# Performance work log

Hardware: AMD Instinct MI355X
Metric: run time of the kernel (lower is better)

The kernel has to match this reference:

```python
import jax, jax.numpy as jnp
import numpy as np

B, T, N = 256, 512, 256
START, STOP = 254, 255


def setup_inputs() -> dict:
    key = jax.random.key(0)
    k1, k2, k3 = jax.random.split(key, 3)
    inputs = jax.random.normal(k1, (B, T, N), dtype=jnp.float32)
    transitions = jax.random.normal(k2, (N, N), dtype=jnp.float32)
    # sentinel rows/cols as in __init__
    transitions = transitions.at[START, :].set(-10000.0).at[:, STOP].set(-10000.0)
    tags = jax.random.randint(k3, (B, T), 0, N, dtype=jnp.int32)
    mask = jnp.ones((B, T), dtype=jnp.int32)
    return {"inputs": inputs, "transitions": transitions, "tags": tags, "mask": mask}


def _input_likelihood(inputs, transitions, fmask):
    # alpha[b, tag]: log-sum over paths ending at tag
    alpha0 = transitions[:, START][None, :] + inputs[:, 0, :]

    def step(alpha, xs):
        emit, m = xs  # emit: (B, N), m: (B,)
        # inner[b, next, prev] = alpha[b, prev] + (emit[b, next] + trans[next, prev]) * mask[b, i-1]
        inner = alpha[:, None, :] + (emit[:, :, None] + transitions[None, :, :]) * m[:, None, None]
        return jax.nn.logsumexp(inner, axis=-1), None

    xs = (jnp.swapaxes(inputs[:, 1:, :], 0, 1), jnp.swapaxes(fmask[:, :-1], 0, 1))
    alpha, _ = jax.lax.scan(step, alpha0, xs)
    stops = alpha + transitions[STOP][None, :]
    return jax.nn.logsumexp(stops, axis=-1)  # (B,)


def _joint_likelihood(inputs, transitions, tags, fmask):
    score = transitions[tags[:, 0], START]  # (B,)
    # transitions[next, prev] * mask[:, i+1], summed over steps
    trans_sc = transitions[tags[:, 1:], tags[:, :-1]] * fmask[:, 1:]
    # inputs[b, i, prev_tag] * mask[:, i]
    emit_sc = jnp.take_along_axis(inputs[:, :-1, :], tags[:, :-1, None], axis=2)[..., 0] * fmask[:, :-1]
    score = score + trans_sc.sum(axis=-1) + emit_sc.sum(axis=-1)
    last_idx = (fmask.sum(axis=-1) - 1.0).astype(jnp.int32)  # (B,)
    last_tags = jnp.take_along_axis(tags, last_idx[:, None], axis=1)[:, 0]
    last_input = jnp.take_along_axis(inputs[:, -1, :], last_tags[:, None], axis=1)[:, 0]
    return score + transitions[STOP, last_tags] + last_input * fmask[:, -1]


def reference(inputs, transitions, tags, mask):
    fmask = mask.astype(jnp.float32)
    log_denominator = _input_likelihood(inputs, transitions, fmask)
    log_numerator = _joint_likelihood(inputs, transitions, tags, fmask)
    return jnp.sum(log_numerator - log_denominator)
```

## Files before the change

### kernel.cpp

```cpp
#include <hip/hip_runtime.h>
#include <hip/hip_bf16.h>
#include <stdint.h>

#define B_    256
#define T_    512
#define N_    256
#define START_ 254
#define STOP_  255
#define GCOLS 16
#define NF    16
#define ND    32
#define LOG2E 1.4426950408889634f
#define LN2   0.6931471805599453f

#define WSB_OFF 65536
#define WCF_OFF 131072
#define WCB_OFF 131328
#define WNUM_OFF 131584

typedef __attribute__((ext_vector_type(4))) float floatx4;
typedef __attribute__((ext_vector_type(4))) unsigned int uintx4;
typedef __attribute__((ext_vector_type(8))) int v8i;

template<bool X> struct BC { static constexpr bool value = X; };

__device__ __forceinline__ void lds_barrier() {
    asm volatile("s_waitcnt lgkmcnt(0)\n\ts_barrier" ::: "memory");
}
__device__ __forceinline__ float fmax3(float a, float b, float c) {
    return fmaxf(fmaxf(a, b), c);
}
__device__ __forceinline__ uint32_t umax32(uint32_t a, uint32_t b) {
    return a > b ? a : b;
}
__device__ __forceinline__ float pmax16(float x) {
    float a = x, b = x;
    asm("v_permlane16_swap_b32 %0, %1" : "+v"(a), "+v"(b));
    return fmaxf(a, b);
}
__device__ __forceinline__ float pmax32(float x) {
    float a = x, b = x;
    asm("v_permlane32_swap_b32 %0, %1" : "+v"(a), "+v"(b));
    return fmaxf(a, b);
}
__device__ __forceinline__ float psum32(float x) {
    float a = x, b = x;
    asm("v_permlane32_swap_b32 %0, %1" : "+v"(a), "+v"(b));
    return a + b;
}

__device__ __forceinline__ int pk_fp8x4(float a, float b, float c, float d) {
    int r = __builtin_amdgcn_cvt_pk_fp8_f32(a, b, 0, false);
    return __builtin_amdgcn_cvt_pk_fp8_f32(c, d, r, true);
}
__device__ __forceinline__ int pk_bf8x4(float a, float b, float c, float d) {
    int r = __builtin_amdgcn_cvt_pk_bf8_f32(a, b, 0, false);
    return __builtin_amdgcn_cvt_pk_bf8_f32(c, d, r, true);
}

struct DenomShared {
    alignas(16) char  V[2][4096];
    alignas(16) unsigned short mbuf[GCOLS * 8];
    alignas(16) float sbuf[GCOLS * 20];
    int flag;
};

template<bool ISF>
__device__ __forceinline__ void denom_path(
    DenomShared& sh, const float* __restrict__ inputs,
    const float* __restrict__ trans, const int* __restrict__ mask,
    float* __restrict__ ws, int blkLocal)
{
    const int tid = threadIdx.x;
    const int w = tid >> 6;
    const int l = tid & 63;
    const int q = l >> 4;
    const int b = l & 15;
    const int bg = blkLocal * GCOLS + b;
    const int j0 = 32 * w + 4 * q;
    const int S = ISF ? 256 : 255;
    const int scl = 0x7F7F7F7F;

    auto EIDX = [](int s) { return ISF ? s : (511 - s); };
    auto MIDX = [](int s) { return ISF ? (s - 1) : (511 - s); };

    int wa[2];
    #pragma unroll
    for (int mt = 0; mt < 2; ++mt)
        wa[mt] = ((((2 * w + mt) >> 3) * 2 + mt) << 10)
               + ((w & 3) << 8) + (b << 4) + (q << 2);
    const int rbase = l << 4;

    v8i afrag[2][2];
    #pragma unroll
    for (int mt = 0; mt < 2; ++mt) {
        const int row = 32 * w + 16 * mt + b;
        #pragma unroll
        for (int c = 0; c < 2; ++c) {
            v8i a;
            #pragma unroll
            for (int g8 = 0; g8 < 8; ++g8) {
                float e[4];
                if (ISF) {
                    floatx4 t = *(const floatx4*)(trans + row * N_ + c * 128 + q * 32 + 4 * g8);
                    #pragma unroll
                    for (int ii = 0; ii < 4; ++ii)
                        e[ii] = __builtin_amdgcn_exp2f(t[ii] * LOG2E);
                } else {
                    #pragma unroll
                    for (int ii = 0; ii < 4; ++ii) {
                        const int k = c * 128 + q * 32 + 4 * g8 + ii;
                        e[ii] = __builtin_amdgcn_exp2f(trans[k * N_ + row] * LOG2E);
                    }
                }
                a[g8] = pk_fp8x4(e[0], e[1], e[2], e[3]);
            }
            afrag[mt][c] = a;
        }
    }

    {
        const int* mrow = mask + blkLocal * GCOLS * T_;
        bool hd = false;
        #pragma unroll
        for (int i = 0; i < GCOLS * T_ / 512; ++i)
            hd |= (mrow[tid + 512 * i] == 0);
        if (tid == 0) sh.flag = 0;
        __syncthreads();
        if (__any(hd) && l == 0) atomicOr(&sh.flag, 1);
        __syncthreads();
    }
    const bool anyDead = (sh.flag != 0);

    const float* emitp = inputs + (size_t)bg * T_ * N_;
    const int*   maskp = mask + bg * T_;
    int   Ci = 0;
    float u[2][4];

    if (ISF) {
        #pragma unroll
        for (int mt = 0; mt < 2; ++mt) {
            floatx4 em = *(const floatx4*)(emitp + j0 + 16 * mt);
            #pragma unroll
            for (int r = 0; r < 4; ++r) {
                const int j = j0 + 16 * mt + r;
                u[mt][r] = __builtin_amdgcn_exp2f((trans[j * N_ + START_] + em[r]) * LOG2E);
            }
        }
    } else {
        #pragma unroll
        for (int mt = 0; mt < 2; ++mt) {
            floatx4 st = *(const floatx4*)(trans + STOP_ * N_ + j0 + 16 * mt);
            #pragma unroll
            for (int r = 0; r < 4; ++r)
                u[mt][r] = __builtin_amdgcn_exp2f(st[r] * LOG2E);
        }
    }
    {
        float mx = u[0][0], sm = 0.f;
        #pragma unroll
        for (int mt = 0; mt < 2; ++mt)
            #pragma unroll
            for (int r = 0; r < 4; ++r) { mx = fmaxf(mx, u[mt][r]); sm += u[mt][r]; }
        mx = pmax16(mx);
        mx = pmax32(mx);
        if (l < 16)
            sh.mbuf[b * 8 + w] =
                (unsigned short)(__builtin_bit_cast(uint32_t, mx) >> 16);
        sm = psum32(sm);
        if (l < 32) sh.sbuf[b * 20 + w * 2 + q] = sm;

        float xpi[2][4] = {{1.f,1.f,1.f,1.f},{1.f,1.f,1.f,1.f}};
        if (!ISF) {
            #pragma unroll
            for (int mt = 0; mt < 2; ++mt) {
                floatx4 e = *(const floatx4*)(emitp + (size_t)511 * N_ + j0 + 16 * mt);
                #pragma unroll
                for (int r = 0; r < 4; ++r)
                    xpi[mt][r] = __builtin_amdgcn_exp2f(e[r] * LOG2E);
            }
        }
        #pragma unroll
        for (int mt = 0; mt < 2; ++mt)
            *(int*)(sh.V[0] + wa[mt]) =
                pk_bf8x4(u[mt][0] * xpi[mt][0], u[mt][1] * xpi[mt][1],
                         u[mt][2] * xpi[mt][2], u[mt][3] * xpi[mt][3]);
    }

    auto run = [&](auto fastc) {
        constexpr bool FAST = decltype(fastc)::value;
        const long estep = ISF ? (long)N_ : -(long)N_;
        const int  mstep = ISF ? 1 : -1;

        floatx4 xc0, xc1;
        floatx4 rbA0, rbA1;
        floatx4 rbB0, rbB1;
        const float* pe = emitp + (size_t)EIDX(1) * N_ + j0;
        {
            floatx4 e0 = *(const floatx4*)pe;
            floatx4 e1 = *(const floatx4*)(pe + 16);
            pe += estep;
            rbA0 = *(const floatx4*)pe;
            rbA1 = *(const floatx4*)(pe + 16);
            pe += estep;
            rbB0 = *(const floatx4*)pe;
            rbB1 = *(const floatx4*)(pe + 16);
            pe += estep;
            #pragma unroll
            for (int r = 0; r < 4; ++r) {
                xc0[r] = __builtin_amdgcn_exp2f(e0[r] * LOG2E);
                xc1[r] = __builtin_amdgcn_exp2f(e1[r] * LOG2E);
            }
        }
        float mrot[2] = {1.f, 1.f};
        const int* pm = maskp;
        if (!FAST) {
            mrot[0] = (float)maskp[MIDX(1)];
            mrot[1] = (float)maskp[MIDX(2)];
            pm = maskp + MIDX(3);
        }
        lds_barrier();

        auto body = [&](int pr, int cur) {
            const char* vb = sh.V[pr];
            uintx4 r00 = *(const uintx4*)(vb + rbase);
            uintx4 r01 = *(const uintx4*)(vb + 1024 + rbase);
            uintx4 r10 = *(const uintx4*)(vb + 2048 + rbase);
            uintx4 r11 = *(const uintx4*)(vb + 3072 + rbase);
            const uintx4 md = *(const uintx4*)((const uint32_t*)sh.mbuf + b * 4);
            floatx4 eC0 = *(const floatx4*)pe;
            floatx4 eC1 = *(const floatx4*)(pe + 16);
            float mC = 1.f;
            if (!FAST) mC = (float)(*pm);

            floatx4 xn0, xn1;
            #pragma unroll
            for (int r = 0; r < 4; ++r) {
                xn0[r] = __builtin_amdgcn_exp2f(rbA0[r] * LOG2E);
                xn1[r] = __builtin_amdgcn_exp2f(rbA1[r] * LOG2E);
            }

            const uint32_t hm = umax32(umax32(md[0], md[1]), umax32(md[2], md[3]));
            const uint32_t lm = umax32(umax32(md[0] << 16, md[1] << 16),
                                       umax32(md[2] << 16, md[3] << 16));
            const uint32_t mm = umax32(hm, lm);
            const int eb = (int)((mm >> 23) & 0xFFu);
            const float rs = __builtin_bit_cast(float, (uint32_t)(249 - eb) << 23);
            Ci += eb;

            floatx4 rx0, rx1;
            if (ISF) {
                #pragma unroll
                for (int r = 0; r < 4; ++r) { rx0[r] = xc0[r] * rs; rx1[r] = xc1[r] * rs; }
            }

            union { v8i v; struct { uintx4 lo, hi; } p; } bf0, bf1;
            bf0.p.lo = r00; bf0.p.hi = r01;
            bf1.p.lo = r10; bf1.p.hi = r11;

            floatx4 a0 = {0.f,0.f,0.f,0.f}, a1 = {0.f,0.f,0.f,0.f};
            a0 = __builtin_amdgcn_mfma_scale_f32_16x16x128_f8f6f4(
                     afrag[0][0], bf0.v, a0, 0, 1, 0, scl, 0, scl);
            a1 = __builtin_amdgcn_mfma_scale_f32_16x16x128_f8f6f4(
                     afrag[1][0], bf0.v, a1, 0, 1, 0, scl, 0, scl);
            a0 = __builtin_amdgcn_mfma_scale_f32_16x16x128_f8f6f4(
                     afrag[0][1], bf1.v, a0, 0, 1, 0, scl, 0, scl);
            a1 = __builtin_amdgcn_mfma_scale_f32_16x16x128_f8f6f4(
                     afrag[1][1], bf1.v, a1, 0, 1, 0, scl, 0, scl);

            if (FAST) {
                #pragma unroll
                for (int r = 0; r < 4; ++r) {
                    if (ISF) {
                        u[0][r] = a0[r] * rx0[r];
                        u[1][r] = a1[r] * rx1[r];
                    } else {
                        u[0][r] = a0[r] * rs;
                        u[1][r] = a1[r] * rs;
                    }
                }
            } else {
                const bool live = (mrot[cur] != 0.f);
                float csv = 0.f;
                if (__any(!live)) {
                    const float* sb = &sh.sbuf[b * 20];
                    floatx4 s0 = *(const floatx4*)sb,       s1 = *(const floatx4*)(sb + 4);
                    floatx4 s2 = *(const floatx4*)(sb + 8), s3 = *(const floatx4*)(sb + 12);
                    csv = ((((s0[0] + s0[1]) + (s0[2] + s0[3])) +
                            ((s1[0] + s1[1]) + (s1[2] + s1[3]))) +
                           (((s2[0] + s2[1]) + (s2[2] + s2[3])) +
                            ((s3[0] + s3[1]) + (s3[2] + s3[3])))) * rs;
                }
                #pragma unroll
                for (int r = 0; r < 4; ++r) {
                    if (ISF) {
                        u[0][r] = live ? a0[r] * rx0[r] : csv;
                        u[1][r] = live ? a1[r] * rx1[r] : csv;
                    } else {
                        u[0][r] = live ? a0[r] * rs : csv;
                        u[1][r] = live ? a1[r] * rs : csv;
                    }
                }
            }

            {
                float t0 = fmax3(u[0][0], u[0][1], u[0][2]);
                t0 = fmax3(t0, u[0][3], u[1][0]);
                t0 = fmax3(t0, u[1][1], u[1][2]);
                t0 = fmaxf(t0, u[1][3]);
                t0 = pmax16(t0);
                t0 = pmax32(t0);
                if (l < 16)
                    sh.mbuf[b * 8 + w] =
                        (unsigned short)(__builtin_bit_cast(uint32_t, t0) >> 16);
                if (!FAST) {
                    float sm = ((u[0][0] + u[0][1]) + (u[0][2] + u[0][3]))
                             + ((u[1][0] + u[1][1]) + (u[1][2] + u[1][3]));
                    sm = psum32(sm);
                    if (l < 32) sh.sbuf[b * 20 + w * 2 + q] = sm;
                }
            }
            if (ISF) {
                *(int*)(sh.V[pr ^ 1] + wa[0]) = pk_bf8x4(u[0][0], u[0][1], u[0][2], u[0][3]);
                *(int*)(sh.V[pr ^ 1] + wa[1]) = pk_bf8x4(u[1][0], u[1][1], u[1][2], u[1][3]);
            } else {
                *(int*)(sh.V[pr ^ 1] + wa[0]) =
                    pk_bf8x4(u[0][0] * xc0[0], u[0][1] * xc0[1],
                             u[0][2] * xc0[2], u[0][3] * xc0[3]);
                *(int*)(sh.V[pr ^ 1] + wa[1]) =
                    pk_bf8x4(u[1][0] * xc1[0], u[1][1] * xc1[1],
                             u[1][2] * xc1[2], u[1][3] * xc1[3]);
            }
            lds_barrier();
            xc0 = xn0; xc1 = xn1;
            rbA0 = rbB0; rbA1 = rbB1;
            rbB0 = eC0;  rbB1 = eC1;
            pe += estep;
            if (!FAST) { mrot[cur] = mC; pm += mstep; }
        };

        #pragma unroll 1
        for (int g = 0; g < S / 2; ++g) {
            body(0, 0);
            body(1, 1);
        }
        if (S & 1) body(0, 0);
    };

    if (anyDead) run(BC<false>{});
    else         run(BC<true>{});

    float* wsV = ws + (ISF ? 0 : WSB_OFF);
    #pragma unroll
    for (int mt = 0; mt < 2; ++mt) {
        floatx4 vv = {u[mt][0], u[mt][1], u[mt][2], u[mt][3]};
        *(floatx4*)&wsV[(size_t)bg * N_ + j0 + 16 * mt] = vv;
    }
    if (tid < 16) {
        float* wsC = ws + (ISF ? WCF_OFF : WCB_OFF);
        wsC[blkLocal * GCOLS + tid] = (float)(Ci - 122 * S);
    }
}

__global__ __launch_bounds__(512, 2) void crf_main(
    const float* __restrict__ inputs, const float* __restrict__ trans,
    const int* __restrict__ tags, const int* __restrict__ mask,
    float* __restrict__ out, float* __restrict__ ws)
{
    __shared__ DenomShared sh;

    if (blockIdx.x >= ND) {
        float* nred = sh.sbuf;
        int*   nredi = (int*)(sh.sbuf + 8);
        const int bb = blockIdx.x - ND;
        const int t  = threadIdx.x;
        const int tg = tags[bb * T_ + t];
        const float fm = (float)mask[bb * T_ + t];
        float part = 0.f;
        if (t >= 1)      part += trans[tg * N_ + tags[bb * T_ + t - 1]] * fm;
        if (t <= T_ - 2) part += inputs[((size_t)bb * T_ + t) * N_ + tg] * fm;
        int ms = mask[bb * T_ + t];
        #pragma unroll
        for (int off = 1; off < 64; off <<= 1) {
            part += __shfl_xor(part, off, 64);
            ms   += __shfl_xor(ms, off, 64);
        }
        if ((t & 63) == 0) { nred[t >> 6] = part; nredi[t >> 6] = ms; }
        __syncthreads();
        if (t == 0) {
            float tot = 0.f; int mtot = 0;
            for (int i = 0; i < 8; ++i) { tot += nred[i]; mtot += nredi[i]; }
            tot += trans[tags[bb * T_] * N_ + START_];
            const int last = mtot - 1;
            const int lt = tags[bb * T_ + last];
            tot += trans[STOP_ * N_ + lt]
                 + inputs[((size_t)bb * T_ + (T_ - 1)) * N_ + lt]
                   * (float)mask[bb * T_ + T_ - 1];
            ws[WNUM_OFF + bb] = tot;
        }
        return;
    }

    if (blockIdx.x < NF) denom_path<true>(sh, inputs, trans, mask, ws, blockIdx.x);
    else                 denom_path<false>(sh, inputs, trans, mask, ws, blockIdx.x - NF);
}

__global__ __launch_bounds__(256) void crf_combine(
    const float* __restrict__ ws, float* __restrict__ out)
{
    __shared__ float red[4];
    const int t = threadIdx.x;
    const int w = t >> 6, l = t & 63;
    float acc = 0.f;
    #pragma unroll 1
    for (int i = 0; i < 4; ++i) {
        const int bb = blockIdx.x * GCOLS + w * 4 + i;
        const float* pa = ws + (size_t)bb * N_;
        const float* pb = ws + WSB_OFF + (size_t)bb * N_;
        floatx4 va = *(const floatx4*)(pa + 4 * l);
        floatx4 vb = *(const floatx4*)(pb + 4 * l);
        float p = va[0] * vb[0] + va[1] * vb[1] + va[2] * vb[2] + va[3] * vb[3];
        #pragma unroll
        for (int off = 1; off < 64; off <<= 1) p += __shfl_xor(p, off, 64);
        if (l == 0) {
            const float denom = (ws[WCF_OFF + bb] + ws[WCB_OFF + bb]
                                 + __builtin_amdgcn_logf(p)) * LN2;
            acc += ws[WNUM_OFF + bb] - denom;
        }
    }
    if (l == 0) red[w] = acc;
    __syncthreads();
    if (t == 0) atomicAdd(out, red[0] + red[1] + red[2] + red[3]);
}

extern "C" void kernel_launch(void* const* d_in, const int* in_sizes, int n_in,
                              void* d_out, int out_size, void* d_ws, size_t ws_size,
                              hipStream_t stream) {
    const float* inputs = (const float*)d_in[0];
    const float* trans  = (const float*)d_in[1];
    const int*   tags   = (const int*)d_in[2];
    const int*   mask   = (const int*)d_in[3];
    float* out = (float*)d_out;
    float* ws  = (float*)d_ws;
    hipMemsetAsync(out, 0, sizeof(float), stream);
    crf_main<<<dim3(ND + B_), dim3(512), 0, stream>>>(inputs, trans, tags, mask, out, ws);
    crf_combine<<<dim3(B_ / GCOLS), dim3(256), 0, stream>>>(ws, out);
}
```

Baseline: 333.1 us.

## Interleave forward and backward CRF recurrences in one block per batch group

Before, separate blocks ran the forward and backward alpha recurrences, 32 denominator blocks in total. Now each of 16 blocks runs both directions, alternating a forward step and a backward step between shared LDS barriers. This halves the number of barriers per step pair and lets the independent MFMA and exp chains of the two directions hide each other's latency on the serial critical path. In exchange it doubles register use for the A-fragments and state, and halves the number of CUs working on the denominator.

```diff
diff --git a/kernel.cpp b/kernel.cpp
--- a/kernel.cpp
+++ b/kernel.cpp
@@ -8,8 +8,7 @@
 #define START_ 254
 #define STOP_  255
 #define GCOLS 16
-#define NF    16
-#define ND    32
+#define NDM   16
 #define LOG2E 1.4426950408889634f
 #define LN2   0.6931471805599453f
 
@@ -59,14 +58,16 @@
 }
 
 struct DenomShared {
-    alignas(16) char  V[2][4096];
-    alignas(16) unsigned short mbuf[GCOLS * 8];
-    alignas(16) float sbuf[GCOLS * 20];
+    alignas(16) char  VF[2][4096];
+    alignas(16) char  VB[2][4096];
+    alignas(16) unsigned short mbufF[GCOLS * 8];
+    alignas(16) unsigned short mbufB[GCOLS * 8];
+    alignas(16) float sbufF[GCOLS * 20];
+    alignas(16) float sbufB[GCOLS * 20];
     int flag;
 };
 
-template<bool ISF>
-__device__ __forceinline__ void denom_path(
+__device__ __forceinline__ void denom_both(
     DenomShared& sh, const float* __restrict__ inputs,
     const float* __restrict__ trans, const int* __restrict__ mask,
     float* __restrict__ ws, int blkLocal)
@@ -78,11 +79,7 @@
     const int b = l & 15;
     const int bg = blkLocal * GCOLS + b;
     const int j0 = 32 * w + 4 * q;
-    const int S = ISF ? 256 : 255;
     const int scl = 0x7F7F7F7F;
-
-    auto EIDX = [](int s) { return ISF ? s : (511 - s); };
-    auto MIDX = [](int s) { return ISF ? (s - 1) : (511 - s); };
 
     int wa[2];
     #pragma unroll
@@ -91,31 +88,28 @@
                + ((w & 3) << 8) + (b << 4) + (q << 2);
     const int rbase = l << 4;
 
-    v8i afrag[2][2];
+    v8i afrag[2][2][2];
     #pragma unroll
     for (int mt = 0; mt < 2; ++mt) {
         const int row = 32 * w + 16 * mt + b;
         #pragma unroll
         for (int c = 0; c < 2; ++c) {
-            v8i a;
+            v8i aF, aB;
             #pragma unroll
             for (int g8 = 0; g8 < 8; ++g8) {
-                float e[4];
-                if (ISF) {
-                    floatx4 t = *(const floatx4*)(trans + row * N_ + c * 128 + q * 32 + 4 * g8);
-                    #pragma unroll
-                    for (int ii = 0; ii < 4; ++ii)
-                        e[ii] = __builtin_amdgcn_exp2f(t[ii] * LOG2E);
-                } else {
-                    #pragma unroll
-                    for (int ii = 0; ii < 4; ++ii) {
-                        const int k = c * 128 + q * 32 + 4 * g8 + ii;
-                        e[ii] = __builtin_amdgcn_exp2f(trans[k * N_ + row] * LOG2E);
-                    }
-                }
-                a[g8] = pk_fp8x4(e[0], e[1], e[2], e[3]);
-            }
-            afrag[mt][c] = a;
+                floatx4 t = *(const floatx4*)(trans + row * N_ + c * 128 + q * 32 + 4 * g8);
+                float eF[4], eB[4];
+                #pragma unroll
+                for (int ii = 0; ii < 4; ++ii) {
+                    eF[ii] = __builtin_amdgcn_exp2f(t[ii] * LOG2E);
+                    const int k = c * 128 + q * 32 + 4 * g8 + ii;
+                    eB[ii] = __builtin_amdgcn_exp2f(trans[k * N_ + row] * LOG2E);
+                }
+                aF[g8] = pk_fp8x4(eF[0], eF[1], eF[2], eF[3]);
+                aB[g8] = pk_fp8x4(eB[0], eB[1], eB[2], eB[3]);
+            }
+            afrag[0][mt][c] = aF;
+            afrag[1][mt][c] = aB;
         }
     }
 
@@ -134,110 +128,132 @@
 
     const float* emitp = inputs + (size_t)bg * T_ * N_;
     const int*   maskp = mask + bg * T_;
-    int   Ci = 0;
-    float u[2][4];
-
-    if (ISF) {
+    int   Ci[2] = {0, 0};
+    float u[2][2][4];
+
+    #pragma unroll
+    for (int mt = 0; mt < 2; ++mt) {
+        floatx4 em = *(const floatx4*)(emitp + j0 + 16 * mt);
+        #pragma unroll
+        for (int r = 0; r < 4; ++r) {
+            const int j = j0 + 16 * mt + r;
+            u[0][mt][r] = __builtin_amdgcn_exp2f((trans[j * N_ + START_] + em[r]) * LOG2E);
+        }
+    }
+    #pragma unroll
+    for (int mt = 0; mt < 2; ++mt) {
+        floatx4 st = *(const floatx4*)(trans + STOP_ * N_ + j0 + 16 * mt);
+        #pragma unroll
+        for (int r = 0; r < 4; ++r)
+            u[1][mt][r] = __builtin_amdgcn_exp2f(st[r] * LOG2E);
+    }
+    {
+        float mx = u[0][0][0], sm = 0.f;
+        #pragma unroll
+        for (int mt = 0; mt < 2; ++mt)
+            #pragma unroll
+            for (int r = 0; r < 4; ++r) { mx = fmaxf(mx, u[0][mt][r]); sm += u[0][mt][r]; }
+        mx = pmax16(mx); mx = pmax32(mx);
+        if (l < 16)
+            sh.mbufF[b * 8 + w] = (unsigned short)(__builtin_bit_cast(uint32_t, mx) >> 16);
+        sm = psum32(sm);
+        if (l < 32) sh.sbufF[b * 20 + w * 2 + q] = sm;
+        #pragma unroll
+        for (int mt = 0; mt < 2; ++mt)
+            *(int*)(sh.VF[0] + wa[mt]) =
+                pk_bf8x4(u[0][mt][0], u[0][mt][1], u[0][mt][2], u[0][mt][3]);
+    }
+    {
+        float mx = u[1][0][0], sm = 0.f;
+        #pragma unroll
+        for (int mt = 0; mt < 2; ++mt)
+            #pragma unroll
+            for (int r = 0; r < 4; ++r) { mx = fmaxf(mx, u[1][mt][r]); sm += u[1][mt][r]; }
+        mx = pmax16(mx); mx = pmax32(mx);
+        if (l < 16)
+            sh.mbufB[b * 8 + w] = (unsigned short)(__builtin_bit_cast(uint32_t, mx) >> 16);
+        sm = psum32(sm);
+        if (l < 32) sh.sbufB[b * 20 + w * 2 + q] = sm;
         #pragma unroll
         for (int mt = 0; mt < 2; ++mt) {
-            floatx4 em = *(const floatx4*)(emitp + j0 + 16 * mt);
-            #pragma unroll
-            for (int r = 0; r < 4; ++r) {
-                const int j = j0 + 16 * mt + r;
-                u[mt][r] = __builtin_amdgcn_exp2f((trans[j * N_ + START_] + em[r]) * LOG2E);
-            }
-        }
-    } else {
-        #pragma unroll
-        for (int mt = 0; mt < 2; ++mt) {
-            floatx4 st = *(const floatx4*)(trans + STOP_ * N_ + j0 + 16 * mt);
-            #pragma unroll
-            for (int r = 0; r < 4; ++r)
-                u[mt][r] = __builtin_amdgcn_exp2f(st[r] * LOG2E);
-        }
-    }
-    {
-        float mx = u[0][0], sm = 0.f;
-        #pragma unroll
-        for (int mt = 0; mt < 2; ++mt)
-            #pragma unroll
-            for (int r = 0; r < 4; ++r) { mx = fmaxf(mx, u[mt][r]); sm += u[mt][r]; }
-        mx = pmax16(mx);
-        mx = pmax32(mx);
-        if (l < 16)
-            sh.mbuf[b * 8 + w] =
-                (unsigned short)(__builtin_bit_cast(uint32_t, mx) >> 16);
-        sm = psum32(sm);
-        if (l < 32) sh.sbuf[b * 20 + w * 2 + q] = sm;
-
-        float xpi[2][4] = {{1.f,1.f,1.f,1.f},{1.f,1.f,1.f,1.f}};
-        if (!ISF) {
-            #pragma unroll
-            for (int mt = 0; mt < 2; ++mt) {
-                floatx4 e = *(const floatx4*)(emitp + (size_t)511 * N_ + j0 + 16 * mt);
-                #pragma unroll
-                for (int r = 0; r < 4; ++r)
-                    xpi[mt][r] = __builtin_amdgcn_exp2f(e[r] * LOG2E);
-            }
-        }
-        #pragma unroll
-        for (int mt = 0; mt < 2; ++mt)
-            *(int*)(sh.V[0] + wa[mt]) =
-                pk_bf8x4(u[mt][0] * xpi[mt][0], u[mt][1] * xpi[mt][1],
-                         u[mt][2] * xpi[mt][2], u[mt][3] * xpi[mt][3]);
+            floatx4 e = *(const floatx4*)(emitp + (size_t)511 * N_ + j0 + 16 * mt);
+            float xp0 = __builtin_amdgcn_exp2f(e[0] * LOG2E);
+            float xp1 = __builtin_amdgcn_exp2f(e[1] * LOG2E);
+            float xp2 = __builtin_amdgcn_exp2f(e[2] * LOG2E);
+            float xp3 = __builtin_amdgcn_exp2f(e[3] * LOG2E);
+            *(int*)(sh.VB[0] + wa[mt]) =
+                pk_bf8x4(u[1][mt][0] * xp0, u[1][mt][1] * xp1,
+                         u[1][mt][2] * xp2, u[1][mt][3] * xp3);
+        }
     }
 
     auto run = [&](auto fastc) {
         constexpr bool FAST = decltype(fastc)::value;
-        const long estep = ISF ? (long)N_ : -(long)N_;
-        const int  mstep = ISF ? 1 : -1;
-
-        floatx4 xc0, xc1;
-        floatx4 rbA0, rbA1;
-        floatx4 rbB0, rbB1;
-        const float* pe = emitp + (size_t)EIDX(1) * N_ + j0;
+
+        floatx4 xc[2][2], ra[2][2];
+        const float* pe[2];
+        const int*   pm[2] = {maskp, maskp};
+        float mrot[2][2] = {{1.f, 1.f}, {1.f, 1.f}};
+
         {
-            floatx4 e0 = *(const floatx4*)pe;
-            floatx4 e1 = *(const floatx4*)(pe + 16);
-            pe += estep;
-            rbA0 = *(const floatx4*)pe;
-            rbA1 = *(const floatx4*)(pe + 16);
-            pe += estep;
-            rbB0 = *(const floatx4*)pe;
-            rbB1 = *(const floatx4*)(pe + 16);
-            pe += estep;
+            const float* p = emitp + (size_t)1 * N_ + j0;
+            floatx4 e0 = *(const floatx4*)p;
+            floatx4 e1 = *(const floatx4*)(p + 16);
+            ra[0][0] = *(const floatx4*)(p + N_);
+            ra[0][1] = *(const floatx4*)(p + N_ + 16);
+            pe[0] = p + 2 * N_;
             #pragma unroll
             for (int r = 0; r < 4; ++r) {
-                xc0[r] = __builtin_amdgcn_exp2f(e0[r] * LOG2E);
-                xc1[r] = __builtin_amdgcn_exp2f(e1[r] * LOG2E);
-            }
-        }
-        float mrot[2] = {1.f, 1.f};
-        const int* pm = maskp;
+                xc[0][0][r] = __builtin_amdgcn_exp2f(e0[r] * LOG2E);
+                xc[0][1][r] = __builtin_amdgcn_exp2f(e1[r] * LOG2E);
+            }
+        }
+        {
+            const float* p = emitp + (size_t)510 * N_ + j0;
+            floatx4 e0 = *(const floatx4*)p;
+            floatx4 e1 = *(const floatx4*)(p + 16);
+            ra[1][0] = *(const floatx4*)(p - N_);
+            ra[1][1] = *(const floatx4*)(p - N_ + 16);
+            pe[1] = p - 2 * N_;
+            #pragma unroll
+            for (int r = 0; r < 4; ++r) {
+                xc[1][0][r] = __builtin_amdgcn_exp2f(e0[r] * LOG2E);
+                xc[1][1][r] = __builtin_amdgcn_exp2f(e1[r] * LOG2E);
+            }
+        }
         if (!FAST) {
-            mrot[0] = (float)maskp[MIDX(1)];
-            mrot[1] = (float)maskp[MIDX(2)];
-            pm = maskp + MIDX(3);
+            mrot[0][0] = (float)maskp[0];
+            mrot[0][1] = (float)maskp[1];
+            pm[0] = maskp + 2;
+            mrot[1][0] = (float)maskp[510];
+            mrot[1][1] = (float)maskp[509];
+            pm[1] = maskp + 508;
         }
         lds_barrier();
 
-        auto body = [&](int pr, int cur) {
-            const char* vb = sh.V[pr];
+        auto step = [&](auto isfc, int pr, int cur) {
+            constexpr bool ISF = decltype(isfc)::value;
+            constexpr int  D = ISF ? 0 : 1;
+            char (*V)[4096] = ISF ? sh.VF : sh.VB;
+            unsigned short* mbufp = ISF ? sh.mbufF : sh.mbufB;
+            const long estep = ISF ? (long)N_ : -(long)N_;
+
+            const char* vb = V[pr];
             uintx4 r00 = *(const uintx4*)(vb + rbase);
             uintx4 r01 = *(const uintx4*)(vb + 1024 + rbase);
             uintx4 r10 = *(const uintx4*)(vb + 2048 + rbase);
             uintx4 r11 = *(const uintx4*)(vb + 3072 + rbase);
-            const uintx4 md = *(const uintx4*)((const uint32_t*)sh.mbuf + b * 4);
-            floatx4 eC0 = *(const floatx4*)pe;
-            floatx4 eC1 = *(const floatx4*)(pe + 16);
+            const uintx4 md = *(const uintx4*)((const uint32_t*)mbufp + b * 4);
+            floatx4 eC0 = *(const floatx4*)pe[D];
+            floatx4 eC1 = *(const floatx4*)(pe[D] + 16);
             float mC = 1.f;
-            if (!FAST) mC = (float)(*pm);
+            if (!FAST) mC = (float)(*pm[D]);
 
             floatx4 xn0, xn1;
             #pragma unroll
             for (int r = 0; r < 4; ++r) {
-                xn0[r] = __builtin_amdgcn_exp2f(rbA0[r] * LOG2E);
-                xn1[r] = __builtin_amdgcn_exp2f(rbA1[r] * LOG2E);
+                xn0[r] = __builtin_amdgcn_exp2f(ra[D][0][r] * LOG2E);
+                xn1[r] = __builtin_amdgcn_exp2f(ra[D][1][r] * LOG2E);
             }
 
             const uint32_t hm = umax32(umax32(md[0], md[1]), umax32(md[2], md[3]));
@@ -246,12 +262,15 @@
             const uint32_t mm = umax32(hm, lm);
             const int eb = (int)((mm >> 23) & 0xFFu);
             const float rs = __builtin_bit_cast(float, (uint32_t)(249 - eb) << 23);
-            Ci += eb;
+            Ci[D] += eb;
 
             floatx4 rx0, rx1;
             if (ISF) {
                 #pragma unroll
-                for (int r = 0; r < 4; ++r) { rx0[r] = xc0[r] * rs; rx1[r] = xc1[r] * rs; }
+                for (int r = 0; r < 4; ++r) {
+                    rx0[r] = xc[0][0][r] * rs;
+                    rx1[r] = xc[0][1][r] * rs;
+                }
             }
 
             union { v8i v; struct { uintx4 lo, hi; } p; } bf0, bf1;
@@ -260,30 +279,30 @@
 
             floatx4 a0 = {0.f,0.f,0.f,0.f}, a1 = {0.f,0.f,0.f,0.f};
             a0 = __builtin_amdgcn_mfma_scale_f32_16x16x128_f8f6f4(
-                     afrag[0][0], bf0.v, a0, 0, 1, 0, scl, 0, scl);
+                     afrag[D][0][0], bf0.v, a0, 0, 1, 0, scl, 0, scl);
             a1 = __builtin_amdgcn_mfma_scale_f32_16x16x128_f8f6f4(
-                     afrag[1][0], bf0.v, a1, 0, 1, 0, scl, 0, scl);
+                     afrag[D][1][0], bf0.v, a1, 0, 1, 0, scl, 0, scl);
             a0 = __builtin_amdgcn_mfma_scale_f32_16x16x128_f8f6f4(
-                     afrag[0][1], bf1.v, a0, 0, 1, 0, scl, 0, scl);
+                     afrag[D][0][1], bf1.v, a0, 0, 1, 0, scl, 0, scl);
             a1 = __builtin_amdgcn_mfma_scale_f32_16x16x128_f8f6f4(
-                     afrag[1][1], bf1.v, a1, 0, 1, 0, scl, 0, scl);
+                     afrag[D][1][1], bf1.v, a1, 0, 1, 0, scl, 0, scl);
 
             if (FAST) {
                 #pragma unroll
                 for (int r = 0; r < 4; ++r) {
                     if (ISF) {
-                        u[0][r] = a0[r] * rx0[r];
-                        u[1][r] = a1[r] * rx1[r];
+                        u[0][0][r] = a0[r] * rx0[r];
+                        u[0][1][r] = a1[r] * rx1[r];
                     } else {
-                        u[0][r] = a0[r] * rs;
-                        u[1][r] = a1[r] * rs;
+                        u[1][0][r] = a0[r] * rs;
+                        u[1][1][r] = a1[r] * rs;
                     }
                 }
             } else {
-                const bool live = (mrot[cur] != 0.f);
+                const bool live = (mrot[D][cur] != 0.f);
                 float csv = 0.f;
                 if (__any(!live)) {
-                    const float* sb = &sh.sbuf[b * 20];
+                    const float* sb = (ISF ? sh.sbufF : sh.sbufB) + b * 20;
                     floatx4 s0 = *(const floatx4*)sb,       s1 = *(const floatx4*)(sb + 4);
                     floatx4 s2 = *(const floatx4*)(sb + 8), s3 = *(const floatx4*)(sb + 12);
                     csv = ((((s0[0] + s0[1]) + (s0[2] + s0[3])) +
@@ -294,71 +313,79 @@
                 #pragma unroll
                 for (int r = 0; r < 4; ++r) {
                     if (ISF) {
-                        u[0][r] = live ? a0[r] * rx0[r] : csv;
-                        u[1][r] = live ? a1[r] * rx1[r] : csv;
+                        u[0][0][r] = live ? a0[r] * rx0[r] : csv;
+                        u[0][1][r] = live ? a1[r] * rx1[r] : csv;
                     } else {
-                        u[0][r] = live ? a0[r] * rs : csv;
-                        u[1][r] = live ? a1[r] * rs : csv;
+                        u[1][0][r] = live ? a0[r] * rs : csv;
+                        u[1][1][r] = live ? a1[r] * rs : csv;
                     }
                 }
             }
 
             {
-                float t0 = fmax3(u[0][0], u[0][1], u[0][2]);
-                t0 = fmax3(t0, u[0][3], u[1][0]);
-                t0 = fmax3(t0, u[1][1], u[1][2]);
-                t0 = fmaxf(t0, u[1][3]);
+                float t0 = fmax3(u[D][0][0], u[D][0][1], u[D][0][2]);
+                t0 = fmax3(t0, u[D][0][3], u[D][1][0]);
+                t0 = fmax3(t0, u[D][1][1], u[D][1][2]);
+                t0 = fmaxf(t0, u[D][1][3]);
                 t0 = pmax16(t0);
                 t0 = pmax32(t0);
                 if (l < 16)
-                    sh.mbuf[b * 8 + w] =
+                    mbufp[b * 8 + w] =
                         (unsigned short)(__builtin_bit_cast(uint32_t, t0) >> 16);
                 if (!FAST) {
-                    float sm = ((u[0][0] + u[0][1]) + (u[0][2] + u[0][3]))
-                             + ((u[1][0] + u[1][1]) + (u[1][2] + u[1][3]));
+                    float sm = ((u[D][0][0] + u[D][0][1]) + (u[D][0][2] + u[D][0][3]))
+                             + ((u[D][1][0] + u[D][1][1]) + (u[D][1][2] + u[D][1][3]));
                     sm = psum32(sm);
-                    if (l < 32) sh.sbuf[b * 20 + w * 2 + q] = sm;
+                    if (l < 32) (ISF ? sh.sbufF : sh.sbufB)[b * 20 + w * 2 + q] = sm;
                 }
             }
             if (ISF) {
-                *(int*)(sh.V[pr ^ 1] + wa[0]) = pk_bf8x4(u[0][0], u[0][1], u[0][2], u[0][3]);
-                *(int*)(sh.V[pr ^ 1] + wa[1]) = pk_bf8x4(u[1][0], u[1][1], u[1][2], u[1][3]);
+                *(int*)(V[pr ^ 1] + wa[0]) =
+                    pk_bf8x4(u[0][0][0], u[0][0][1], u[0][0][2], u[0][0][3]);
+                *(int*)(V[pr ^ 1] + wa[1]) =
+                    pk_bf8x4(u[0][1][0], u[0][1][1], u[0][1][2], u[0][1][3]);
             } else {
-                *(int*)(sh.V[pr ^ 1] + wa[0]) =
-                    pk_bf8x4(u[0][0] * xc0[0], u[0][1] * xc0[1],
-                             u[0][2] * xc0[2], u[0][3] * xc0[3]);
-                *(int*)(sh.V[pr ^ 1] + wa[1]) =
-                    pk_bf8x4(u[1][0] * xc1[0], u[1][1] * xc1[1],
-                             u[1][2] * xc1[2], u[1][3] * xc1[3]);
-            }
+                *(int*)(V[pr ^ 1] + wa[0]) =
+                    pk_bf8x4(u[1][0][0] * xc[1][0][0], u[1][0][1] * xc[1][0][1],
+                             u[1][0][2] * xc[1][0][2], u[1][0][3] * xc[1][0][3]);
+                *(int*)(V[pr ^ 1] + wa[1]) =
+                    pk_bf8x4(u[1][1][0] * xc[1][1][0], u[1][1][1] * xc[1][1][1],
+                             u[1][1][2] * xc[1][1][2], u[1][1][3] * xc[1][1][3]);
+            }
+            xc[D][0] = xn0; xc[D][1] = xn1;
+            ra[D][0] = eC0; ra[D][1] = eC1;
+            pe[D] += estep;
+            if (!FAST) { mrot[D][cur] = mC; pm[D] += ISF ? 1 : -1; }
+        };
+
+        #pragma unroll 1
+        for (int g = 0; g < 127; ++g) {
+            step(BC<true>{}, 0, 0);
+            step(BC<false>{}, 0, 0);
             lds_barrier();
-            xc0 = xn0; xc1 = xn1;
-            rbA0 = rbB0; rbA1 = rbB1;
-            rbB0 = eC0;  rbB1 = eC1;
-            pe += estep;
-            if (!FAST) { mrot[cur] = mC; pm += mstep; }
-        };
-
-        #pragma unroll 1
-        for (int g = 0; g < S / 2; ++g) {
-            body(0, 0);
-            body(1, 1);
-        }
-        if (S & 1) body(0, 0);
+            step(BC<true>{}, 1, 1);
+            step(BC<false>{}, 1, 1);
+            lds_barrier();
+        }
+        step(BC<true>{}, 0, 0);
+        step(BC<false>{}, 0, 0);
+        lds_barrier();
+        step(BC<true>{}, 1, 1);
     };
 
     if (anyDead) run(BC<false>{});
     else         run(BC<true>{});
 
-    float* wsV = ws + (ISF ? 0 : WSB_OFF);
     #pragma unroll
     for (int mt = 0; mt < 2; ++mt) {
-        floatx4 vv = {u[mt][0], u[mt][1], u[mt][2], u[mt][3]};
-        *(floatx4*)&wsV[(size_t)bg * N_ + j0 + 16 * mt] = vv;
+        floatx4 vf = {u[0][mt][0], u[0][mt][1], u[0][mt][2], u[0][mt][3]};
+        *(floatx4*)&ws[(size_t)bg * N_ + j0 + 16 * mt] = vf;
+        floatx4 vbb = {u[1][mt][0], u[1][mt][1], u[1][mt][2], u[1][mt][3]};
+        *(floatx4*)&ws[WSB_OFF + (size_t)bg * N_ + j0 + 16 * mt] = vbb;
     }
     if (tid < 16) {
-        float* wsC = ws + (ISF ? WCF_OFF : WCB_OFF);
-        wsC[blkLocal * GCOLS + tid] = (float)(Ci - 122 * S);
+        ws[WCF_OFF + blkLocal * GCOLS + tid] = (float)(Ci[0] - 122 * 256);
+        ws[WCB_OFF + blkLocal * GCOLS + tid] = (float)(Ci[1] - 122 * 255);
     }
 }
 
@@ -369,10 +396,10 @@
 {
     __shared__ DenomShared sh;
 
-    if (blockIdx.x >= ND) {
-        float* nred = sh.sbuf;
-        int*   nredi = (int*)(sh.sbuf + 8);
-        const int bb = blockIdx.x - ND;
+    if (blockIdx.x >= NDM) {
+        float* nred = sh.sbufF;
+        int*   nredi = (int*)(sh.sbufF + 8);
+        const int bb = blockIdx.x - NDM;
         const int t  = threadIdx.x;
         const int tg = tags[bb * T_ + t];
         const float fm = (float)mask[bb * T_ + t];
@@ -401,8 +428,7 @@
         return;
     }
 
-    if (blockIdx.x < NF) denom_path<true>(sh, inputs, trans, mask, ws, blockIdx.x);
-    else                 denom_path<false>(sh, inputs, trans, mask, ws, blockIdx.x - NF);
+    denom_both(sh, inputs, trans, mask, ws, blockIdx.x);
 }
 
 __global__ __launch_bounds__(256) void crf_combine(
@@ -443,6 +469,6 @@
     float* out = (float*)d_out;
     float* ws  = (float*)d_ws;
     hipMemsetAsync(out, 0, sizeof(float), stream);
-    crf_main<<<dim3(ND + B_), dim3(512), 0, stream>>>(inputs, trans, tags, mask, out, ws);
+    crf_main<<<dim3(NDM + B_), dim3(512), 0, stream>>>(inputs, trans, tags, mask, out, ws);
     crf_combine<<<dim3(B_ / GCOLS), dim3(256), 0, stream>>>(ws, out);
 }
```

After: 449.5 us. 1.35x slower.
